# Kernel tuning notes

Hardware: AMD Instinct MI355X
Metric: run time of the kernel (lower is better)

## Reference

```python
import jax, jax.numpy as jnp
import numpy as np

EPS = 1e-8
PROB_PENALTY = 1e-4
REV_SCALE = 0.1


def _barycenters(vertices, faces):
    # vertices: [N,3], faces: [F,3] int -> [F,3]
    return vertices[faces].mean(axis=1)


def _pairwise_sq_dists(a, b):
    # a: [P,3], b: [Q,3] -> [P,Q] squared euclidean distances via dot expansion
    a2 = jnp.sum(a * a, axis=-1)  # [P]
    b2 = jnp.sum(b * b, axis=-1)  # [Q]
    return a2[:, None] + b2[None, :] - 2.0 * (a @ b.T)


def setup_inputs() -> dict:
    key = jax.random.key(0)
    k_ov, k_of, k_sv, k_sf, k_fp, k_u1, k_u2 = jax.random.split(key, 7)
    N_ORIG, F_ORIG = 8000, 16000
    N_SIMP, F_SIMP = 2500, 4000
    NUM_SAMPLES = 8
    return {
        "original_vertices": jax.random.normal(k_ov, (N_ORIG, 3), dtype=jnp.float32),
        "original_faces": jax.random.randint(k_of, (F_ORIG, 3), 0, N_ORIG, dtype=jnp.int64) if jax.config.jax_enable_x64 else jax.random.randint(k_of, (F_ORIG, 3), 0, N_ORIG, dtype=jnp.int32),
        "simplified_vertices": jax.random.normal(k_sv, (N_SIMP, 3), dtype=jnp.float32),
        "simplified_faces": jax.random.randint(k_sf, (F_SIMP, 3), 0, N_SIMP, dtype=jnp.int32),
        "face_probabilities": jax.random.uniform(k_fp, (F_SIMP,), dtype=jnp.float32),
        "u1": jax.random.uniform(k_u1, (F_SIMP, NUM_SAMPLES, 1), dtype=jnp.float32),
        "u2": jax.random.uniform(k_u2, (F_SIMP, NUM_SAMPLES, 1), dtype=jnp.float32),
    }


def reference(original_vertices, original_faces, simplified_vertices,
              simplified_faces, face_probabilities, u1, u2):
    num_samples = u1.shape[1]

    # ---- forward term: simplified barycenters -> nearest original barycenter ----
    simp_bc = _barycenters(simplified_vertices, simplified_faces)  # [Fs,3]
    orig_bc = _barycenters(original_vertices, original_faces)      # [Fo,3]
    min_d2 = jnp.min(_pairwise_sq_dists(simp_bc, orig_bc), axis=1)  # [Fs]
    forward_term = jnp.sum(face_probabilities * min_d2) \
        + PROB_PENALTY * jnp.sum(1.0 - face_probabilities)

    # ---- reverse term: sample points on simplified triangles, 1-NN to original verts ----
    fv = simplified_vertices[simplified_faces]  # [Fs,3(verts),3(xyz)]
    r1 = jnp.sqrt(u1)                           # [Fs,S,1]
    a = 1.0 - r1
    b = r1 * (1.0 - u2)
    c = r1 * u2
    samples = (a * fv[:, None, 0] + b * fv[:, None, 1] + c * fv[:, None, 2])  # [Fs,S,3]
    pts = samples.reshape(-1, 3)  # [Fs*S,3]

    # brute-force 1-NN squared distances (pytorch3d knn convention)
    min_dist = jnp.min(_pairwise_sq_dists(pts, original_vertices), axis=1)  # [Fs*S]
    scaled = (min_dist / (jnp.max(min_dist) + EPS)) * REV_SCALE
    fp_expanded = jnp.repeat(face_probabilities, num_samples)  # [Fs*S]
    reverse_term = jnp.sum(fp_expanded * scaled)

    return forward_term + reverse_term
```

## Files before the change

### kernel.cpp

```cpp
#include <hip/hip_runtime.h>

#define EPSF 1e-8f
#define PROB_PENALTYF 1e-4f
#define REV_SCALEF 0.1f
#define INFBITS 0x7F800000u
#define ONEBF ((unsigned short)0x3F80)
#define SENT_C 1.0e6f

#define PTW 4
#define WPB 4
#define CS 64
#define NG 8
#define FBLK 256

typedef __attribute__((ext_vector_type(8))) short short8;
typedef __attribute__((ext_vector_type(4))) float f32x4;

__device__ __forceinline__ float min3f(float a, float b, float c) {
    return fminf(fminf(a, b), c);
}

__device__ __forceinline__ unsigned short bfh(float f) {
    unsigned u = __float_as_uint(f);
    return (unsigned short)((u + 0x7FFFu + ((u >> 16) & 1u)) >> 16);
}
__device__ __forceinline__ float bftof(unsigned short h) {
    return __uint_as_float(((unsigned)h) << 16);
}
__device__ __forceinline__ unsigned short bfl(float f, unsigned short h) {
    return bfh(f - bftof(h));
}
__device__ __forceinline__ unsigned pk(unsigned short lo, unsigned short hi) {
    return (unsigned)lo | ((unsigned)hi << 16);
}

__device__ __forceinline__ uint4 makeAfrag(float x, float y, float z, float w, int g) {
    unsigned short hx = bfh(x), hy = bfh(y), hz = bfh(z);
    uint4 r;
    if (g == 0) {
        unsigned short lx = bfl(x, hx), ly = bfl(y, hy), lz = bfl(z, hz);
        r.x = pk(hx, hy); r.y = pk(hz, lx); r.z = pk(ly, lz); r.w = pk(hx, hy);
    } else {
        unsigned short hw = bfh(w), lw = bfl(w, hw);
        r.x = pk(hz, ONEBF); r.y = pk(ONEBF, hw); r.z = pk(lw, 0); r.w = 0u;
    }
    return r;
}
__device__ __forceinline__ uint4 makeBfrag(float x, float y, float z, float w, int g) {
    unsigned short hx = bfh(x), hy = bfh(y), hz = bfh(z);
    uint4 r;
    if (g == 0) {
        unsigned short lx = bfl(x, hx), ly = bfl(y, hy);
        r.x = pk(hx, hy); r.y = pk(hz, hx); r.z = pk(hy, hz); r.w = pk(lx, ly);
    } else {
        unsigned short lz = bfl(z, hz);
        unsigned short hw = bfh(w), lw = bfl(w, hw);
        r.x = pk(lz, hw); r.y = pk(lw, ONEBF); r.z = pk(ONEBF, 0); r.w = 0u;
    }
    return r;
}

__global__ void prep_kernel(const float* __restrict__ overts,
                            const int* __restrict__ ofaces,
                            const float* __restrict__ sverts,
                            const int* __restrict__ sfaces,
                            const float* __restrict__ u1,
                            const float* __restrict__ u2,
                            uint4* __restrict__ revA, uint4* __restrict__ fwdA,
                            uint4* __restrict__ revB, uint4* __restrict__ fwdB,
                            unsigned* __restrict__ rev_min,
                            unsigned* __restrict__ fwd_min,
                            float* __restrict__ acc,
                            int n_orig, int f_orig, int fs, int S, int npts,
                            int revPt, int fwdPt, int revSt, int fwdSt) {
    int tid = blockIdx.x * blockDim.x + threadIdx.x;
    const float third = 1.0f / 3.0f;
    int r0 = revPt * 32, r1 = r0 + fwdPt * 32, r2 = r1 + revSt * 32, r3 = r2 + fwdSt * 32;

    if (tid < r0) {
        int l = tid & 31, g = l >> 4;
        int k = (tid >> 5) * 16 + (l & 15);
        float x = 0.f, y = 0.f, z = 0.f;
        if (k < npts) {
            int f = k / S;
            float rr = sqrtf(u1[k]);
            float uu = u2[k];
            float wa = 1.0f - rr, wb = rr * (1.0f - uu), wc = rr * uu;
            int a = sfaces[3 * f], b = sfaces[3 * f + 1], c = sfaces[3 * f + 2];
            x = wa * sverts[3 * a] + wb * sverts[3 * b] + wc * sverts[3 * c];
            y = wa * sverts[3 * a + 1] + wb * sverts[3 * b + 1] + wc * sverts[3 * c + 1];
            z = wa * sverts[3 * a + 2] + wb * sverts[3 * b + 2] + wc * sverts[3 * c + 2];
        }
        float p2 = x * x + y * y + z * z;
        revA[tid] = makeAfrag(-2.f * x, -2.f * y, -2.f * z, p2, g);
    } else if (tid < r1) {
        int t2 = tid - r0;
        int l = t2 & 31, g = l >> 4;
        int k = (t2 >> 5) * 16 + (l & 15);
        float x = 0.f, y = 0.f, z = 0.f;
        if (k < fs) {
            int a = sfaces[3 * k], b = sfaces[3 * k + 1], c = sfaces[3 * k + 2];
            x = (sverts[3 * a] + sverts[3 * b] + sverts[3 * c]) * third;
            y = (sverts[3 * a + 1] + sverts[3 * b + 1] + sverts[3 * c + 1]) * third;
            z = (sverts[3 * a + 2] + sverts[3 * b + 2] + sverts[3 * c + 2]) * third;
        }
        float p2 = x * x + y * y + z * z;
        fwdA[t2] = makeAfrag(-2.f * x, -2.f * y, -2.f * z, p2, g);
    } else if (tid < r2) {
        int t2 = tid - r1;
        int l = t2 & 31, g = l >> 4;
        int s = (t2 >> 5) * 16 + (l & 15);
        float x = SENT_C, y = SENT_C, z = SENT_C;
        if (s < n_orig) { x = overts[3 * s]; y = overts[3 * s + 1]; z = overts[3 * s + 2]; }
        revB[t2] = makeBfrag(x, y, z, x * x + y * y + z * z, g);
    } else if (tid < r3) {
        int t2 = tid - r2;
        int l = t2 & 31, g = l >> 4;
        int s = (t2 >> 5) * 16 + (l & 15);
        float x = SENT_C, y = SENT_C, z = SENT_C;
        if (s < f_orig) {
            int a = ofaces[3 * s], b = ofaces[3 * s + 1], c = ofaces[3 * s + 2];
            x = (overts[3 * a] + overts[3 * b] + overts[3 * c]) * third;
            y = (overts[3 * a + 1] + overts[3 * b + 1] + overts[3 * c + 1]) * third;
            z = (overts[3 * a + 2] + overts[3 * b + 2] + overts[3 * c + 2]) * third;
        }
        fwdB[t2] = makeBfrag(x, y, z, x * x + y * y + z * z, g);
    } else {
        int t2 = tid - r3;
        if (t2 < npts) rev_min[t2] = INFBITS;
        if (t2 < fs)   fwd_min[t2] = INFBITS;
        if (t2 < 8)    acc[t2] = 0.0f;
    }
}

__global__ void __launch_bounds__(256, 4)
mfma_min_kernel(const uint4* __restrict__ revA, const uint4* __restrict__ fwdA,
                const uint4* __restrict__ revB, const uint4* __restrict__ fwdB,
                unsigned* __restrict__ rev_min, unsigned* __restrict__ fwd_min,
                int revGroups, int revWaves, int revPt, int revNpts, int revSt,
                int fwdGroups, int fwdPt, int fwdNpts, int fwdSt) {
    __shared__ short8 lds[2][NG * 32];
    int tid = (int)threadIdx.x;
    int gw = blockIdx.x * WPB + (tid >> 6);
    int lane = tid & 63;

    const uint4 *A, *B;
    unsigned* omin;
    int group, chunk, nTile, npts, nst;
    if (gw < revWaves) {
        A = revA; B = revB; omin = rev_min; nTile = revPt; npts = revNpts; nst = revSt;
        group = gw % revGroups; chunk = gw / revGroups;
    } else {
        int g2 = gw - revWaves;
        A = fwdA; B = fwdB; omin = fwd_min; nTile = fwdPt; npts = fwdNpts; nst = fwdSt;
        group = g2 % fwdGroups; chunk = g2 / fwdGroups;
    }
    int s0 = chunk * CS;

    const short8* A8 = reinterpret_cast<const short8*>(A);
    const short8* B8 = reinterpret_cast<const short8*>(B);

    const short8 zero8 = {0, 0, 0, 0, 0, 0, 0, 0};
    short8 a[PTW];
    int pt0 = group * PTW;
    #pragma unroll
    for (int r = 0; r < PTW; ++r) {
        int ptile = min(pt0 + r, nTile - 1);
        short8 av = A8[(size_t)ptile * 32 + (lane & 31)];
        a[r] = (lane < 32) ? av : zero8;
    }

    float inf = __uint_as_float(INFBITS);
    f32x4 m[PTW];
    #pragma unroll
    for (int r = 0; r < PTW; ++r) m[r] = (f32x4){inf, inf, inf, inf};
    f32x4 cz = {0.f, 0.f, 0.f, 0.f};

    {
        int gtile = min(s0 + (tid >> 5), nst - 1);
        lds[0][tid] = B8[(size_t)gtile * 32 + (tid & 31)];
    }
    __syncthreads();

    int cur = 0;
    for (int g = 0; g < NG; ++g) {
        short8 vn;
        if (g + 1 < NG) {
            int gtile = min(s0 + (g + 1) * 8 + (tid >> 5), nst - 1);
            vn = B8[(size_t)gtile * 32 + (tid & 31)];
        }
        #pragma unroll
        for (int lt = 0; lt < 8; lt += 2) {
            short8 b0 = lds[cur][lt * 32 + (lane & 31)];
            short8 b1 = lds[cur][(lt + 1) * 32 + (lane & 31)];
            #pragma unroll
            for (int r = 0; r < PTW; ++r) {
                f32x4 d0 = __builtin_amdgcn_mfma_f32_16x16x32_bf16(a[r], b0, cz, 0, 0, 0);
                f32x4 d1 = __builtin_amdgcn_mfma_f32_16x16x32_bf16(a[r], b1, cz, 0, 0, 0);
                m[r].x = min3f(m[r].x, d0.x, d1.x);
                m[r].y = min3f(m[r].y, d0.y, d1.y);
                m[r].z = min3f(m[r].z, d0.z, d1.z);
                m[r].w = min3f(m[r].w, d0.w, d1.w);
            }
        }
        if (g + 1 < NG) {
            lds[cur ^ 1][tid] = vn;
        }
        __syncthreads();
        cur ^= 1;
    }

    #pragma unroll
    for (int off = 1; off < 16; off <<= 1) {
        #pragma unroll
        for (int r = 0; r < PTW; ++r) {
            m[r].x = fminf(m[r].x, __shfl_xor(m[r].x, off));
            m[r].y = fminf(m[r].y, __shfl_xor(m[r].y, off));
            m[r].z = fminf(m[r].z, __shfl_xor(m[r].z, off));
            m[r].w = fminf(m[r].w, __shfl_xor(m[r].w, off));
        }
    }

    if ((lane & 15) == 0) {
        int rowbase = (lane >> 4) * 4;
        #pragma unroll
        for (int r = 0; r < PTW; ++r) {
            int pb = min(pt0 + r, nTile - 1) * 16 + rowbase;
            if (pb + 0 < npts) atomicMin(&omin[pb + 0], __float_as_uint(fmaxf(m[r].x, 0.f)));
            if (pb + 1 < npts) atomicMin(&omin[pb + 1], __float_as_uint(fmaxf(m[r].y, 0.f)));
            if (pb + 2 < npts) atomicMin(&omin[pb + 2], __float_as_uint(fmaxf(m[r].z, 0.f)));
            if (pb + 3 < npts) atomicMin(&omin[pb + 3], __float_as_uint(fmaxf(m[r].w, 0.f)));
        }
    }
}

__global__ void finalize_kernel(const unsigned int* __restrict__ fwd_min,
                                const unsigned int* __restrict__ rev_min,
                                const float* __restrict__ fp,
                                float* acc, float* out,
                                int fs, int npts, int S, int nblocks) {
    __shared__ float s1[FBLK], s2[FBLK], s3[FBLK];
    int k = blockIdx.x * blockDim.x + threadIdx.x;
    float fsum = 0.f, rsum = 0.f, rmax = 0.f;
    if (k < npts) {
        float md = __uint_as_float(rev_min[k]);
        float p = fp[k / S];
        rsum = p * md;
        rmax = md;
    }
    if (k < fs) {
        float p = fp[k];
        fsum = p * __uint_as_float(fwd_min[k]) + PROB_PENALTYF * (1.0f - p);
    }
    s1[threadIdx.x] = fsum;
    s2[threadIdx.x] = rsum;
    s3[threadIdx.x] = rmax;
    __syncthreads();
    for (int off = FBLK / 2; off > 0; off >>= 1) {
        if ((int)threadIdx.x < off) {
            s1[threadIdx.x] += s1[threadIdx.x + off];
            s2[threadIdx.x] += s2[threadIdx.x + off];
            s3[threadIdx.x] = fmaxf(s3[threadIdx.x], s3[threadIdx.x + off]);
        }
        __syncthreads();
    }
    if (threadIdx.x == 0) {
        atomicAdd(&acc[0], s1[0]);
        atomicAdd(&acc[1], s2[0]);
        atomicMax((unsigned int*)&acc[2], __float_as_uint(s3[0]));
        __threadfence();
        unsigned int ticket = atomicAdd((unsigned int*)&acc[3], 1u);
        if (ticket == (unsigned int)(nblocks - 1)) {
            __threadfence();
            float a0 = atomicAdd(&acc[0], 0.0f);
            float a1 = atomicAdd(&acc[1], 0.0f);
            unsigned int mb = atomicOr((unsigned int*)&acc[2], 0u);
            out[0] = a0 + a1 * (REV_SCALEF / (__uint_as_float(mb) + EPSF));
        }
    }
}

extern "C" void kernel_launch(void* const* d_in, const int* in_sizes, int n_in,
                              void* d_out, int out_size, void* d_ws, size_t ws_size,
                              hipStream_t stream) {
    const float* overts = (const float*)d_in[0];
    const int*   ofaces = (const int*)d_in[1];
    const float* sverts = (const float*)d_in[2];
    const int*   sfaces = (const int*)d_in[3];
    const float* fp     = (const float*)d_in[4];
    const float* u1     = (const float*)d_in[5];
    const float* u2     = (const float*)d_in[6];
    float* out = (float*)d_out;

    const int N_ORIG = in_sizes[0] / 3;
    const int F_ORIG = in_sizes[1] / 3;
    const int F_SIMP = in_sizes[3] / 3;
    const int S      = in_sizes[5] / F_SIMP;
    const int NPTS   = F_SIMP * S;

    const int revPt = (NPTS + 15) / 16;
    const int fwdPt = (F_SIMP + 15) / 16;
    const int revSt = (N_ORIG + 15) / 16;
    const int fwdSt = (F_ORIG + 15) / 16;

    uint4* revA = (uint4*)d_ws;
    uint4* fwdA = revA + (size_t)revPt * 32;
    uint4* revB = fwdA + (size_t)fwdPt * 32;
    uint4* fwdB = revB + (size_t)revSt * 32;
    unsigned* rev_min = (unsigned*)(fwdB + (size_t)fwdSt * 32);
    unsigned* fwd_min = rev_min + NPTS;
    float* acc = (float*)(fwd_min + F_SIMP);

    int prepThreads = (revPt + fwdPt + revSt + fwdSt) * 32 + NPTS;
    hipLaunchKernelGGL(prep_kernel, dim3((prepThreads + 255) / 256), dim3(256), 0, stream,
                       overts, ofaces, sverts, sfaces, u1, u2,
                       revA, fwdA, revB, fwdB, rev_min, fwd_min, acc,
                       N_ORIG, F_ORIG, F_SIMP, S, NPTS,
                       revPt, fwdPt, revSt, fwdSt);

    const int revGroups = (((revPt + PTW - 1) / PTW + 3) & ~3);
    const int revChunks = (revSt + CS - 1) / CS;
    const int revWaves = revGroups * revChunks;

    const int fwdGroups = (((fwdPt + PTW - 1) / PTW + 3) & ~3);
    const int fwdChunks = (fwdSt + CS - 1) / CS;
    const int fwdWaves = fwdGroups * fwdChunks;

    const int totalWaves = revWaves + fwdWaves;
    const int mblocks = totalWaves / WPB;
    hipLaunchKernelGGL(mfma_min_kernel, dim3(mblocks), dim3(256), 0, stream,
                       revA, fwdA, revB, fwdB, rev_min, fwd_min,
                       revGroups, revWaves, revPt, NPTS, revSt,
                       fwdGroups, fwdPt, F_SIMP, fwdSt);

    const int finBlocks = (NPTS + FBLK - 1) / FBLK;
    hipLaunchKernelGGL(finalize_kernel, dim3(finBlocks), dim3(FBLK), 0, stream,
                       fwd_min, rev_min, fp, acc, out, F_SIMP, NPTS, S, finBlocks);
}
```

Before: 40.76 us.

## Drop LDS staging of B tiles, halve per-wave point tiles, raise occupancy

Removes the double-buffered shared-memory staging of the B fragments and the per-group block barriers. Each wave now loads its B tiles straight from global memory, relying on L1/L2 for reuse across waves. PTW drops from 4 to 2, which roughly doubles the number of waves and lowers register pressure, and the launch bound now asks for 8 blocks per CU. The cost is more global/cache load traffic per MFMA and less reuse of each B tile across point tiles. Group padding is removed and the block count is rounded up; waves beyond the fwd range in the last block appear to go unguarded.

```diff
diff --git a/kernel.cpp b/kernel.cpp
--- a/kernel.cpp
+++ b/kernel.cpp
@@ -7,10 +7,9 @@
 #define ONEBF ((unsigned short)0x3F80)
 #define SENT_C 1.0e6f
 
-#define PTW 4
+#define PTW 2
 #define WPB 4
 #define CS 64
-#define NG 8
 #define FBLK 256
 
 typedef __attribute__((ext_vector_type(8))) short short8;
@@ -133,13 +132,12 @@
     }
 }
 
-__global__ void __launch_bounds__(256, 4)
+__global__ void __launch_bounds__(256, 8)
 mfma_min_kernel(const uint4* __restrict__ revA, const uint4* __restrict__ fwdA,
                 const uint4* __restrict__ revB, const uint4* __restrict__ fwdB,
                 unsigned* __restrict__ rev_min, unsigned* __restrict__ fwd_min,
                 int revGroups, int revWaves, int revPt, int revNpts, int revSt,
                 int fwdGroups, int fwdPt, int fwdNpts, int fwdSt) {
-    __shared__ short8 lds[2][NG * 32];
     int tid = (int)threadIdx.x;
     int gw = blockIdx.x * WPB + (tid >> 6);
     int lane = tid & 63;
@@ -158,79 +156,67 @@
     int s0 = chunk * CS;
 
     const short8* A8 = reinterpret_cast<const short8*>(A);
-    const short8* B8 = reinterpret_cast<const short8*>(B);
+    const short8* B8 = reinterpret_cast<const short8*>(B) + (lane & 31);
 
     const short8 zero8 = {0, 0, 0, 0, 0, 0, 0, 0};
-    short8 a[PTW];
+    short8 a0, a1;
     int pt0 = group * PTW;
-    #pragma unroll
-    for (int r = 0; r < PTW; ++r) {
-        int ptile = min(pt0 + r, nTile - 1);
-        short8 av = A8[(size_t)ptile * 32 + (lane & 31)];
-        a[r] = (lane < 32) ? av : zero8;
+    {
+        int p0 = min(pt0, nTile - 1);
+        int p1 = min(pt0 + 1, nTile - 1);
+        short8 v0 = A8[(size_t)p0 * 32 + (lane & 31)];
+        short8 v1 = A8[(size_t)p1 * 32 + (lane & 31)];
+        a0 = (lane < 32) ? v0 : zero8;
+        a1 = (lane < 32) ? v1 : zero8;
     }
 
     float inf = __uint_as_float(INFBITS);
-    f32x4 m[PTW];
-    #pragma unroll
-    for (int r = 0; r < PTW; ++r) m[r] = (f32x4){inf, inf, inf, inf};
+    f32x4 m0 = {inf, inf, inf, inf}, m1 = m0;
     f32x4 cz = {0.f, 0.f, 0.f, 0.f};
 
-    {
-        int gtile = min(s0 + (tid >> 5), nst - 1);
-        lds[0][tid] = B8[(size_t)gtile * 32 + (tid & 31)];
-    }
-    __syncthreads();
-
-    int cur = 0;
-    for (int g = 0; g < NG; ++g) {
-        short8 vn;
-        if (g + 1 < NG) {
-            int gtile = min(s0 + (g + 1) * 8 + (tid >> 5), nst - 1);
-            vn = B8[(size_t)gtile * 32 + (tid & 31)];
-        }
-        #pragma unroll
-        for (int lt = 0; lt < 8; lt += 2) {
-            short8 b0 = lds[cur][lt * 32 + (lane & 31)];
-            short8 b1 = lds[cur][(lt + 1) * 32 + (lane & 31)];
-            #pragma unroll
-            for (int r = 0; r < PTW; ++r) {
-                f32x4 d0 = __builtin_amdgcn_mfma_f32_16x16x32_bf16(a[r], b0, cz, 0, 0, 0);
-                f32x4 d1 = __builtin_amdgcn_mfma_f32_16x16x32_bf16(a[r], b1, cz, 0, 0, 0);
-                m[r].x = min3f(m[r].x, d0.x, d1.x);
-                m[r].y = min3f(m[r].y, d0.y, d1.y);
-                m[r].z = min3f(m[r].z, d0.z, d1.z);
-                m[r].w = min3f(m[r].w, d0.w, d1.w);
-            }
-        }
-        if (g + 1 < NG) {
-            lds[cur ^ 1][tid] = vn;
-        }
-        __syncthreads();
-        cur ^= 1;
+    for (int s = 0; s < CS; s += 2) {
+        int g0 = min(s0 + s, nst - 1);
+        int g1 = min(s0 + s + 1, nst - 1);
+        short8 b0 = B8[(size_t)g0 * 32];
+        short8 b1 = B8[(size_t)g1 * 32];
+        f32x4 d00 = __builtin_amdgcn_mfma_f32_16x16x32_bf16(a0, b0, cz, 0, 0, 0);
+        f32x4 d01 = __builtin_amdgcn_mfma_f32_16x16x32_bf16(a0, b1, cz, 0, 0, 0);
+        f32x4 d10 = __builtin_amdgcn_mfma_f32_16x16x32_bf16(a1, b0, cz, 0, 0, 0);
+        f32x4 d11 = __builtin_amdgcn_mfma_f32_16x16x32_bf16(a1, b1, cz, 0, 0, 0);
+        m0.x = min3f(m0.x, d00.x, d01.x);
+        m0.y = min3f(m0.y, d00.y, d01.y);
+        m0.z = min3f(m0.z, d00.z, d01.z);
+        m0.w = min3f(m0.w, d00.w, d01.w);
+        m1.x = min3f(m1.x, d10.x, d11.x);
+        m1.y = min3f(m1.y, d10.y, d11.y);
+        m1.z = min3f(m1.z, d10.z, d11.z);
+        m1.w = min3f(m1.w, d10.w, d11.w);
     }
 
     #pragma unroll
     for (int off = 1; off < 16; off <<= 1) {
-        #pragma unroll
-        for (int r = 0; r < PTW; ++r) {
-            m[r].x = fminf(m[r].x, __shfl_xor(m[r].x, off));
-            m[r].y = fminf(m[r].y, __shfl_xor(m[r].y, off));
-            m[r].z = fminf(m[r].z, __shfl_xor(m[r].z, off));
-            m[r].w = fminf(m[r].w, __shfl_xor(m[r].w, off));
-        }
+        m0.x = fminf(m0.x, __shfl_xor(m0.x, off));
+        m0.y = fminf(m0.y, __shfl_xor(m0.y, off));
+        m0.z = fminf(m0.z, __shfl_xor(m0.z, off));
+        m0.w = fminf(m0.w, __shfl_xor(m0.w, off));
+        m1.x = fminf(m1.x, __shfl_xor(m1.x, off));
+        m1.y = fminf(m1.y, __shfl_xor(m1.y, off));
+        m1.z = fminf(m1.z, __shfl_xor(m1.z, off));
+        m1.w = fminf(m1.w, __shfl_xor(m1.w, off));
     }
 
     if ((lane & 15) == 0) {
         int rowbase = (lane >> 4) * 4;
-        #pragma unroll
-        for (int r = 0; r < PTW; ++r) {
-            int pb = min(pt0 + r, nTile - 1) * 16 + rowbase;
-            if (pb + 0 < npts) atomicMin(&omin[pb + 0], __float_as_uint(fmaxf(m[r].x, 0.f)));
-            if (pb + 1 < npts) atomicMin(&omin[pb + 1], __float_as_uint(fmaxf(m[r].y, 0.f)));
-            if (pb + 2 < npts) atomicMin(&omin[pb + 2], __float_as_uint(fmaxf(m[r].z, 0.f)));
-            if (pb + 3 < npts) atomicMin(&omin[pb + 3], __float_as_uint(fmaxf(m[r].w, 0.f)));
-        }
+        int pb0 = min(pt0, nTile - 1) * 16 + rowbase;
+        int pb1 = min(pt0 + 1, nTile - 1) * 16 + rowbase;
+        if (pb0 + 0 < npts) atomicMin(&omin[pb0 + 0], __float_as_uint(fmaxf(m0.x, 0.f)));
+        if (pb0 + 1 < npts) atomicMin(&omin[pb0 + 1], __float_as_uint(fmaxf(m0.y, 0.f)));
+        if (pb0 + 2 < npts) atomicMin(&omin[pb0 + 2], __float_as_uint(fmaxf(m0.z, 0.f)));
+        if (pb0 + 3 < npts) atomicMin(&omin[pb0 + 3], __float_as_uint(fmaxf(m0.w, 0.f)));
+        if (pb1 + 0 < npts) atomicMin(&omin[pb1 + 0], __float_as_uint(fmaxf(m1.x, 0.f)));
+        if (pb1 + 1 < npts) atomicMin(&omin[pb1 + 1], __float_as_uint(fmaxf(m1.y, 0.f)));
+        if (pb1 + 2 < npts) atomicMin(&omin[pb1 + 2], __float_as_uint(fmaxf(m1.z, 0.f)));
+        if (pb1 + 3 < npts) atomicMin(&omin[pb1 + 3], __float_as_uint(fmaxf(m1.w, 0.f)));
     }
 }
 
@@ -318,16 +304,16 @@
                        N_ORIG, F_ORIG, F_SIMP, S, NPTS,
                        revPt, fwdPt, revSt, fwdSt);
 
-    const int revGroups = (((revPt + PTW - 1) / PTW + 3) & ~3);
+    const int revGroups = (revPt + PTW - 1) / PTW;
     const int revChunks = (revSt + CS - 1) / CS;
     const int revWaves = revGroups * revChunks;
 
-    const int fwdGroups = (((fwdPt + PTW - 1) / PTW + 3) & ~3);
+    const int fwdGroups = (fwdPt + PTW - 1) / PTW;
     const int fwdChunks = (fwdSt + CS - 1) / CS;
     const int fwdWaves = fwdGroups * fwdChunks;
 
     const int totalWaves = revWaves + fwdWaves;
-    const int mblocks = totalWaves / WPB;
+    const int mblocks = (totalWaves + WPB - 1) / WPB;
     hipLaunchKernelGGL(mfma_min_kernel, dim3(mblocks), dim3(256), 0, stream,
                        revA, fwdA, revB, fwdB, rev_min, fwd_min,
                        revGroups, revWaves, revPt, NPTS, revSt,
```

New measurement: 45.81 us. 12.4% more time.
